# Optimization experiments

Hardware: AMD Instinct MI355X
Metric: run time of the kernel (lower is better)

Reference implementation:

```python
import jax, jax.numpy as jnp
import numpy as np

NLON = 720  # output longitude points for irfft
B, C = 4, 8
LMAX, MMAX, NLAT = 360, 361, 361


def setup_inputs() -> dict:
    key = jax.random.key(0)
    kx, kd = jax.random.split(key)
    # x: real view of complex coeffs, shape [B, C, 2(vec comp), lmax, mmax, 2(re/im)]
    x = jax.random.normal(kx, (B, C, 2, LMAX, MMAX, 2), dtype=jnp.float32)
    # dpct: precomputed dLegendre buffer, shape [2, mmax, lmax, nlat]
    dpct = jax.random.normal(kd, (2, MMAX, LMAX, NLAT), dtype=jnp.float32) * 0.1
    return {"x": x, "dpct": dpct}


def reference(x, dpct):
    # split vector components and real/imag parts
    x0r = x[..., 0, :, :, 0]  # [..., lmax, mmax]
    x0i = x[..., 0, :, :, 1]
    x1r = x[..., 1, :, :, 0]
    x1i = x[..., 1, :, :, 1]
    d0 = dpct[0].astype(x.dtype)  # [mmax, lmax, nlat]
    d1 = dpct[1].astype(x.dtype)

    def ein(a, d):
        return jnp.einsum('...lm,mlk->...km', a, d)

    srl = ein(x0r, d0) - ein(x1i, d1)   # [..., nlat, mmax]
    sim = ein(x0i, d0) + ein(x1r, d1)
    trl = -ein(x0i, d1) - ein(x1r, d0)
    tim = ein(x0r, d1) - ein(x1i, d0)

    s = jax.lax.complex(srl, sim)
    t = jax.lax.complex(trl, tim)
    xs = jnp.stack((s, t), axis=-3)     # [..., 2, nlat, mmax] complex
    # inverse real FFT over longitude, 'forward' norm (no scaling on inverse)
    out = jnp.fft.irfft(xs, n=NLON, axis=-1, norm='forward')  # [..., 2, nlat, nlon]
    return out
```

## Files before the change

kernel.cpp:

```cpp
#include <hip/hip_runtime.h>
#include <hip/hip_bf16.h>
#include <math.h>

#define LMAX 360
#define MMAX 361
#define NLAT 361
#define NLON 720
#define BC   32
#define MT   (BC*2*NLAT)
#define QT   722
#define KP   736
#define NP   768
#define BM   128
#define BN   128
#define BK   32

typedef __attribute__((ext_vector_type(8))) short short8;
typedef __attribute__((ext_vector_type(4))) float f32x4;

static __device__ __forceinline__ short f2bf(float v) {
    __hip_bfloat16 h = __float2bfloat16(v);
    return *reinterpret_cast<short*>(&h);
}

__global__ __launch_bounds__(256) void sht_prep_x(
    const float* __restrict__ x, __hip_bfloat16* __restrict__ xT)
{
    const int m0 = blockIdx.x * 32;
    const int l0 = blockIdx.y * 64;
    const int bc = blockIdx.z >> 1, f = blockIdx.z & 1;
    __shared__ float2 tile[64][33];
    const float2* __restrict__ x2 = (const float2*)x;
    const int t = threadIdx.x;
    const int rm = t & 31, rl = t >> 5;

    const int mm = min(m0 + rm, MMAX - 1);
    #pragma unroll
    for (int r = 0; r < 8; ++r) {
        int l = min(l0 + rl + r * 8, LMAX - 1);
        tile[rl + r * 8][rm] = x2[((size_t)(bc * 2 + f) * LMAX + l) * MMAX + mm];
    }
    __syncthreads();

    const int tm = t >> 3, lg = t & 7;
    const int m = m0 + tm;
    if (m >= MMAX) return;
    const int lw = l0 + lg * 8;
    if (lw >= LMAX) return;

    short8 re, im;
    #pragma unroll
    for (int e = 0; e < 8; ++e) {
        float2 v = tile[lg * 8 + e][tm];
        re[e] = f2bf(v.x);
        im[e] = f2bf(v.y);
    }
    size_t mb = (size_t)m * (128 * LMAX);
    *(short8*)((short*)xT + mb + (size_t)((f * 2 + 0) * 32 + bc) * LMAX + lw) = re;
    *(short8*)((short*)xT + mb + (size_t)((f * 2 + 1) * 32 + bc) * LMAX + lw) = im;
}

__global__ __launch_bounds__(256, 3) void sht_gemm1(
    const float* __restrict__ dpct, const __hip_bfloat16* __restrict__ xT,
    __hip_bfloat16* __restrict__ interQ)
{
    const int m  = blockIdx.x;
    const int K0 = blockIdx.y * 96;

    __shared__ __align__(16) char AlsB[96 * 128];
    __shared__ __align__(16) char BlsB[128 * 128];

    const int t    = threadIdx.x;
    const int lane = t & 63;
    const int wave = t >> 6;
    const int wm = (wave >> 1) * 48;
    const int wn = (wave & 1) * 64;
    const int fr = lane & 15;
    const int lq = lane >> 4;

    int kdv[3], lov[3], kcl[3];
    #pragma unroll
    for (int it = 0; it < 3; ++it) {
        int task = it * 256 + t;
        kdv[it] = task % 96;
        lov[it] = task / 96;
        kcl[it] = min(K0 + kdv[it], 360);
    }
    const int cB    = t >> 1;
    const int plane = cB >> 5, bcq = cB & 31;
    const int g0B   = (t & 1) * 4;

    const int            srcT[8] = {0, 1, 2, 3, 3, 2, 1, 0};
    const unsigned short sgnT[8] = {0, 0, 0x8000, 0x8000, 0x8000, 0, 0x8000, 0};

    f32x4 acc[3][4];
    const f32x4 zero = {0.f, 0.f, 0.f, 0.f};
    #pragma unroll
    for (int i = 0; i < 3; ++i)
        #pragma unroll
        for (int j = 0; j < 4; ++j) acc[i][j] = zero;

    float  apf[3][8];
    short8 bpf[4];
    bool   lvA[3], bvB[4];
    short  bsgn = 0;

    auto loadA = [&](int p, int l0) {
        const size_t rowb = ((size_t)p * MMAX + m) * LMAX;
        #pragma unroll
        for (int it = 0; it < 3; ++it) {
            int lb = l0 + lov[it] * 8;
            lvA[it] = (lb < LMAX);
            int lcl = lvA[it] ? lb : 0;
            const float* src = dpct + (rowb + lcl) * (size_t)NLAT + kcl[it];
            #pragma unroll
            for (int e = 0; e < 8; ++e)
                apf[it][e] = src[(size_t)e * NLAT];
        }
    };

    auto loadB = [&](int p, int l0) {
        int src = srcT[p * 4 + plane];
        bsgn = (short)sgnT[p * 4 + plane];
        const short* bbase = (const short*)xT + (size_t)m * (128 * LMAX) +
                             (size_t)(src * 32 + bcq) * LMAX;
        #pragma unroll
        for (int i = 0; i < 4; ++i) {
            int lg2 = l0 + (g0B + i) * 8;
            bvB[i] = (lg2 < LMAX);
            int lcl = bvB[i] ? lg2 : 0;
            bpf[i] = *(const short8*)(bbase + lcl);
        }
    };

    auto writeA = [&]() {
        #pragma unroll
        for (int it = 0; it < 3; ++it) {
            short8 w;
            #pragma unroll
            for (int e = 0; e < 8; ++e)
                w[e] = lvA[it] ? f2bf(apf[it][e]) : (short)0;
            int kd = kdv[it], lo = lov[it];
            *(short8*)(AlsB + kd * 128 + ((lo ^ (kd & 7)) << 4)) = w;
        }
    };

    auto writeB = [&]() {
        #pragma unroll
        for (int i = 0; i < 4; ++i) {
            short8 v = bpf[i];
            #pragma unroll
            for (int e = 0; e < 8; ++e) {
                short xe = (short)(v[e] ^ bsgn);
                v[e] = bvB[i] ? xe : (short)0;
            }
            int g = g0B + i;
            *(short8*)(BlsB + cB * 128 + ((g ^ (cB & 7)) << 4)) = v;
        }
    };

    loadA(0, 0);
    loadB(0, 0);

    #pragma unroll 1
    for (int s = 0; s < 12; ++s) {
        __syncthreads();
        writeA();
        writeB();
        __syncthreads();

        if (s < 11) {
            const int pn  = (s + 1 >= 6) ? 1 : 0;
            const int l0n = ((s + 1) % 6) * 64;
            loadA(pn, l0n);
            loadB(pn, l0n);
        }

        #pragma unroll
        for (int kk = 0; kk < 2; ++kk) {
            short8 af[3], bg[4];
            const int g = kk * 4 + lq;
            #pragma unroll
            for (int mi = 0; mi < 3; ++mi) {
                int k = wm + mi * 16 + fr;
                af[mi] = *(const short8*)(AlsB + k * 128 + ((g ^ (k & 7)) << 4));
            }
            #pragma unroll
            for (int ni = 0; ni < 4; ++ni) {
                int c = wn + ni * 16 + fr;
                bg[ni] = *(const short8*)(BlsB + c * 128 + ((g ^ (c & 7)) << 4));
            }
            #pragma unroll
            for (int mi = 0; mi < 3; ++mi)
                #pragma unroll
                for (int ni = 0; ni < 4; ++ni)
                    acc[mi][ni] = __builtin_amdgcn_mfma_f32_16x16x32_bf16(
                        af[mi], bg[ni], acc[mi][ni], 0, 0, 0);
        }
    }

    #pragma unroll
    for (int mi = 0; mi < 3; ++mi) {
        int kr = K0 + wm + mi * 16 + lq * 4;
        #pragma unroll
        for (int ni = 0; ni < 4; ++ni) {
            int c = wn + ni * 16 + fr;
            int pl = c >> 5, bc = c & 31;
            int ri = pl & 1, tt = pl >> 1;
            size_t qb = (size_t)(2 * m + ri) * MT + (size_t)(bc * 2 + tt) * NLAT;
            #pragma unroll
            for (int r = 0; r < 4; ++r) {
                int k = kr + r;
                if (k < NLAT)
                    interQ[qb + k] = __float2bfloat16(acc[mi][ni][r]);
            }
        }
    }
}

__global__ __launch_bounds__(256) void sht_transpose(
    const __hip_bfloat16* __restrict__ inQ, __hip_bfloat16* __restrict__ outT)
{
    __shared__ __hip_bfloat16 tile[64][65];
    const int R0 = blockIdx.x * 64;
    const int q0 = blockIdx.y * 64;
    const int tx = threadIdx.x & 63;
    const int ty = threadIdx.x >> 6;
    const __hip_bfloat16 zv = __float2bfloat16(0.f);

    for (int qq = ty; qq < 64; qq += 4) {
        int q = q0 + qq;
        tile[qq][tx] = (q < QT) ? inQ[(size_t)q * MT + R0 + tx] : zv;
    }
    __syncthreads();
    if (q0 + tx < KP) {
        for (int rr = ty; rr < 64; rr += 4) {
            outT[(size_t)(R0 + rr) * KP + q0 + tx] = tile[tx][rr];
        }
    }
}

__global__ __launch_bounds__(256) void sht_make_w(__hip_bfloat16* __restrict__ W)
{
    const int idx = blockIdx.x * 256 + threadIdx.x;
    const int j = idx / KP;
    const int q = idx % KP;
    float v = 0.f;
    if (j < NLON && q < QT) {
        int m = q >> 1;
        float coef = (m == 0 || m == 360) ? 1.f : 2.f;
        int ph = (m * j) % 720;
        float ang = (float)ph * (float)(2.0 * M_PI / 720.0);
        float s, c;
        __sincosf(ang, &s, &c);
        v = (q & 1) ? (-coef * s) : (coef * c);
    }
    W[idx] = __float2bfloat16(v);
}

__global__ __launch_bounds__(256) void sht_gemm(
    const __hip_bfloat16* __restrict__ A,
    const __hip_bfloat16* __restrict__ W,
    float* __restrict__ out)
{
    __shared__ __align__(16) __hip_bfloat16 As[BM * BK];
    __shared__ __align__(16) __hip_bfloat16 Bs[BN * BK];
    const int t  = threadIdx.x;
    const int R0 = blockIdx.x * BM;
    const int J0 = blockIdx.y * BN;

    const int rowA = t >> 2;
    const int kc   = (t & 3) * 8;
    const int gr0  = min(R0 + rowA,      MT - 1);
    const int gr1  = min(R0 + rowA + 64, MT - 1);
    const __hip_bfloat16* pa0 = A + (size_t)gr0 * KP + kc;
    const __hip_bfloat16* pa1 = A + (size_t)gr1 * KP + kc;
    const __hip_bfloat16* pb0 = W + (size_t)(J0 + rowA) * KP + kc;
    const __hip_bfloat16* pb1 = W + (size_t)(J0 + rowA + 64) * KP + kc;

    const int lane = t & 63;
    const int wave = t >> 6;
    const int wm = (wave >> 1) * 64;
    const int wn = (wave & 1) * 64;
    const int fr = lane & 15;
    const int kg = (lane >> 4) * 8;

    f32x4 acc[4][4];
    const f32x4 zero = {0.f, 0.f, 0.f, 0.f};
    #pragma unroll
    for (int i = 0; i < 4; ++i)
        #pragma unroll
        for (int j = 0; j < 4; ++j) acc[i][j] = zero;

    short8 va0 = *(const short8*)pa0;
    short8 va1 = *(const short8*)pa1;
    short8 vb0 = *(const short8*)pb0;
    short8 vb1 = *(const short8*)pb1;

    for (int kt = 0; kt < KP / BK; ++kt) {
        __syncthreads();
        *(short8*)&As[t * 8]        = va0;
        *(short8*)&As[t * 8 + 2048] = va1;
        *(short8*)&Bs[t * 8]        = vb0;
        *(short8*)&Bs[t * 8 + 2048] = vb1;
        __syncthreads();

        if (kt + 1 < KP / BK) {
            const int ko = (kt + 1) * BK;
            va0 = *(const short8*)(pa0 + ko);
            va1 = *(const short8*)(pa1 + ko);
            vb0 = *(const short8*)(pb0 + ko);
            vb1 = *(const short8*)(pb1 + ko);
        }

        short8 af[4], bg[4];
        #pragma unroll
        for (int i = 0; i < 4; ++i)
            af[i] = *(const short8*)&As[(wm + i * 16 + fr) * BK + kg];
        #pragma unroll
        for (int i = 0; i < 4; ++i)
            bg[i] = *(const short8*)&Bs[(wn + i * 16 + fr) * BK + kg];

        #pragma unroll
        for (int mi = 0; mi < 4; ++mi)
            #pragma unroll
            for (int ni = 0; ni < 4; ++ni)
                acc[mi][ni] = __builtin_amdgcn_mfma_f32_16x16x32_bf16(
                    af[mi], bg[ni], acc[mi][ni], 0, 0, 0);
    }

    const int orow = (lane >> 4) * 4;
    #pragma unroll
    for (int mi = 0; mi < 4; ++mi) {
        #pragma unroll
        for (int ni = 0; ni < 4; ++ni) {
            #pragma unroll
            for (int r = 0; r < 4; ++r) {
                int row = R0 + wm + mi * 16 + orow + r;
                int col = J0 + wn + ni * 16 + fr;
                if (row < MT && col < NLON)
                    out[(size_t)row * NLON + col] = acc[mi][ni][r];
            }
        }
    }
}

extern "C" void kernel_launch(void* const* d_in, const int* in_sizes, int n_in,
                              void* d_out, int out_size, void* d_ws, size_t ws_size,
                              hipStream_t stream)
{
    const float* x    = (const float*)d_in[0];
    const float* dpct = (const float*)d_in[1];
    float* out        = (float*)d_out;

    char* ws = (char*)d_ws;
    __hip_bfloat16* xT     = (__hip_bfloat16*)ws;
    __hip_bfloat16* interT = (__hip_bfloat16*)ws;
    __hip_bfloat16* interQ = (__hip_bfloat16*)(ws + 34009088);
    __hip_bfloat16* Wt     = (__hip_bfloat16*)(ws + 34009088);

    dim3 gp(12, 6, 64);
    sht_prep_x<<<gp, 256, 0, stream>>>(x, xT);

    dim3 g1(MMAX, 4);
    sht_gemm1<<<g1, 256, 0, stream>>>(dpct, xT, interQ);

    dim3 gt(MT / 64, 12);
    sht_transpose<<<gt, 256, 0, stream>>>(interQ, interT);

    sht_make_w<<<(NP * KP) / 256, 256, 0, stream>>>(Wt);

    dim3 gg((MT + BM - 1) / BM, NP / BN);
    sht_gemm<<<gg, 256, 0, stream>>>(interT, Wt, out);
}
```

Measured before the change: 273.6 us.

## Pre-convert dpct to padded transposed bf16 layout before the first GEMM

Adds a kernel that reads the fp32 Legendre table, converts it to bf16 and writes it transposed into a zero-padded [p][m][k][l] workspace layout. The first GEMM then loads A tiles as contiguous 16-byte vectors with no per-element conversion or bounds masks, replacing eight strided scalar fp32 loads per thread. Occupancy hint is raised to 4 blocks per CU. This adds a full extra pass over dpct (read fp32, write bf16) every call, so the saving in the GEMM has to exceed the cost of the new kernel.

```diff
diff --git a/kernel.cpp b/kernel.cpp
--- a/kernel.cpp
+++ b/kernel.cpp
@@ -14,6 +14,8 @@
 #define BM   128
 #define BN   128
 #define BK   32
+#define KD4  384
+#define LD4  384
 
 typedef __attribute__((ext_vector_type(8))) short short8;
 typedef __attribute__((ext_vector_type(4))) float f32x4;
@@ -60,8 +62,53 @@
     *(short8*)((short*)xT + mb + (size_t)((f * 2 + 1) * 32 + bc) * LMAX + lw) = im;
 }
 
-__global__ __launch_bounds__(256, 3) void sht_gemm1(
-    const float* __restrict__ dpct, const __hip_bfloat16* __restrict__ xT,
+__global__ __launch_bounds__(256) void sht_conv_dpct(
+    const float* __restrict__ dpct, __hip_bfloat16* __restrict__ dpctT)
+{
+    const int g = blockIdx.x;
+    const int m = blockIdx.y;
+    const int p = blockIdx.z;
+    const int t = threadIdx.x;
+    const bool zpad = (g == 15);
+
+    __shared__ float raw[24 * NLAT];
+
+    if (!zpad) {
+        const float4* __restrict__ src4 = (const float4*)(
+            dpct + ((size_t)(p * MMAX + m) * LMAX + g * 24) * NLAT);
+        float4* raw4 = (float4*)raw;
+        #pragma unroll
+        for (int i = 0; i < 9; ++i) {
+            int idx = i * 256 + t;
+            if (idx < 2166) raw4[idx] = src4[idx];
+        }
+    }
+    __syncthreads();
+
+    short* __restrict__ dstb = (short*)dpctT +
+        ((size_t)(p * MMAX + m) * KD4) * LD4 + g * 24;
+
+    #pragma unroll
+    for (int i = 0; i < 5; ++i) {
+        int task = i * 256 + t;
+        if (task >= 1152) break;
+        int k  = task / 3;
+        int sh = task % 3;
+        short8 w;
+        if (!zpad && k <= 360) {
+            #pragma unroll
+            for (int e = 0; e < 8; ++e)
+                w[e] = f2bf(raw[(sh * 8 + e) * NLAT + k]);
+        } else {
+            #pragma unroll
+            for (int e = 0; e < 8; ++e) w[e] = 0;
+        }
+        *(short8*)(dstb + (size_t)k * LD4 + sh * 8) = w;
+    }
+}
+
+__global__ __launch_bounds__(256, 4) void sht_gemm1(
+    const __hip_bfloat16* __restrict__ dpctT, const __hip_bfloat16* __restrict__ xT,
     __hip_bfloat16* __restrict__ interQ)
 {
     const int m  = blockIdx.x;
@@ -78,13 +125,12 @@
     const int fr = lane & 15;
     const int lq = lane >> 4;
 
-    int kdv[3], lov[3], kcl[3];
+    int kdv[3], lgv[3];
     #pragma unroll
     for (int it = 0; it < 3; ++it) {
         int task = it * 256 + t;
-        kdv[it] = task % 96;
-        lov[it] = task / 96;
-        kcl[it] = min(K0 + kdv[it], 360);
+        kdv[it] = task >> 3;
+        lgv[it] = task & 7;
     }
     const int cB    = t >> 1;
     const int plane = cB >> 5, bcq = cB & 31;
@@ -100,30 +146,25 @@
         #pragma unroll
         for (int j = 0; j < 4; ++j) acc[i][j] = zero;
 
-    float  apf[3][8];
+    short8 apf[3];
     short8 bpf[4];
-    bool   lvA[3], bvB[4];
+    bool   bvB[4];
     short  bsgn = 0;
 
+    const short* __restrict__ abase = (const short*)dpctT;
+    const short* __restrict__ xbase = (const short*)xT + (size_t)m * (128 * LMAX);
+
     auto loadA = [&](int p, int l0) {
-        const size_t rowb = ((size_t)p * MMAX + m) * LMAX;
-        #pragma unroll
-        for (int it = 0; it < 3; ++it) {
-            int lb = l0 + lov[it] * 8;
-            lvA[it] = (lb < LMAX);
-            int lcl = lvA[it] ? lb : 0;
-            const float* src = dpct + (rowb + lcl) * (size_t)NLAT + kcl[it];
-            #pragma unroll
-            for (int e = 0; e < 8; ++e)
-                apf[it][e] = src[(size_t)e * NLAT];
-        }
+        const short* sl = abase + ((size_t)(p * MMAX + m) * KD4 + K0) * LD4 + l0;
+        #pragma unroll
+        for (int it = 0; it < 3; ++it)
+            apf[it] = *(const short8*)(sl + (size_t)kdv[it] * LD4 + lgv[it] * 8);
     };
 
     auto loadB = [&](int p, int l0) {
         int src = srcT[p * 4 + plane];
         bsgn = (short)sgnT[p * 4 + plane];
-        const short* bbase = (const short*)xT + (size_t)m * (128 * LMAX) +
-                             (size_t)(src * 32 + bcq) * LMAX;
+        const short* bbase = xbase + (size_t)(src * 32 + bcq) * LMAX;
         #pragma unroll
         for (int i = 0; i < 4; ++i) {
             int lg2 = l0 + (g0B + i) * 8;
@@ -136,12 +177,8 @@
     auto writeA = [&]() {
         #pragma unroll
         for (int it = 0; it < 3; ++it) {
-            short8 w;
-            #pragma unroll
-            for (int e = 0; e < 8; ++e)
-                w[e] = lvA[it] ? f2bf(apf[it][e]) : (short)0;
-            int kd = kdv[it], lo = lov[it];
-            *(short8*)(AlsB + kd * 128 + ((lo ^ (kd & 7)) << 4)) = w;
+            int kd = kdv[it], lg = lgv[it];
+            *(short8*)(AlsB + kd * 128 + ((lg ^ (kd & 7)) << 4)) = apf[it];
         }
     };
 
@@ -358,12 +395,16 @@
     __hip_bfloat16* interT = (__hip_bfloat16*)ws;
     __hip_bfloat16* interQ = (__hip_bfloat16*)(ws + 34009088);
     __hip_bfloat16* Wt     = (__hip_bfloat16*)(ws + 34009088);
+    __hip_bfloat16* dpctT  = (__hip_bfloat16*)(ws + 67371264);
 
     dim3 gp(12, 6, 64);
     sht_prep_x<<<gp, 256, 0, stream>>>(x, xT);
 
+    dim3 gc(16, MMAX, 2);
+    sht_conv_dpct<<<gc, 256, 0, stream>>>(dpct, dpctT);
+
     dim3 g1(MMAX, 4);
-    sht_gemm1<<<g1, 256, 0, stream>>>(dpct, xT, interQ);
+    sht_gemm1<<<g1, 256, 0, stream>>>(dpctT, xT, interQ);
 
     dim3 gt(MT / 64, 12);
     sht_transpose<<<gt, 256, 0, stream>>>(interQ, interT);
```

Result: slower. 432.5 us (+58.1%).

## Double-buffer register prefetch of A/B tiles two steps ahead in GEMM loop

Applied to the files above, without the earlier changes.

Adds a second set of register staging buffers so global loads for step s+2 are issued while step s is written to LDS and computed, deepening the prefetch from one step to two. The loop is unrolled by two to alternate between the buffers. This aims to hide the strided global loads of dpct behind more MFMA work, at the cost of roughly doubling staging register use, which may reduce occupancy or cause spills.

```diff
diff --git a/kernel.cpp b/kernel.cpp
--- a/kernel.cpp
+++ b/kernel.cpp
@@ -100,12 +100,12 @@
         #pragma unroll
         for (int j = 0; j < 4; ++j) acc[i][j] = zero;
 
-    float  apf[3][8];
-    short8 bpf[4];
-    bool   lvA[3], bvB[4];
-    short  bsgn = 0;
-
-    auto loadA = [&](int p, int l0) {
+    float  apf0[3][8], apf1[3][8];
+    short8 bpf0[4],    bpf1[4];
+    bool   lvA0[3], lvA1[3], bvB0[4], bvB1[4];
+    short  bsgn0 = 0, bsgn1 = 0;
+
+    auto loadA = [&](float (*apf)[8], bool* lvA, int p, int l0) {
         const size_t rowb = ((size_t)p * MMAX + m) * LMAX;
         #pragma unroll
         for (int it = 0; it < 3; ++it) {
@@ -119,7 +119,7 @@
         }
     };
 
-    auto loadB = [&](int p, int l0) {
+    auto loadB = [&](short8* bpf, bool* bvB, short& bsgn, int p, int l0) {
         int src = srcT[p * 4 + plane];
         bsgn = (short)sgnT[p * 4 + plane];
         const short* bbase = (const short*)xT + (size_t)m * (128 * LMAX) +
@@ -133,7 +133,7 @@
         }
     };
 
-    auto writeA = [&]() {
+    auto writeA = [&](const float (*apf)[8], const bool* lvA) {
         #pragma unroll
         for (int it = 0; it < 3; ++it) {
             short8 w;
@@ -145,7 +145,7 @@
         }
     };
 
-    auto writeB = [&]() {
+    auto writeB = [&](const short8* bpf, const bool* bvB, short bsgn) {
         #pragma unroll
         for (int i = 0; i < 4; ++i) {
             short8 v = bpf[i];
@@ -159,23 +159,7 @@
         }
     };
 
-    loadA(0, 0);
-    loadB(0, 0);
-
-    #pragma unroll 1
-    for (int s = 0; s < 12; ++s) {
-        __syncthreads();
-        writeA();
-        writeB();
-        __syncthreads();
-
-        if (s < 11) {
-            const int pn  = (s + 1 >= 6) ? 1 : 0;
-            const int l0n = ((s + 1) % 6) * 64;
-            loadA(pn, l0n);
-            loadB(pn, l0n);
-        }
-
+    auto compute = [&]() {
         #pragma unroll
         for (int kk = 0; kk < 2; ++kk) {
             short8 af[3], bg[4];
@@ -197,7 +181,40 @@
                     acc[mi][ni] = __builtin_amdgcn_mfma_f32_16x16x32_bf16(
                         af[mi], bg[ni], acc[mi][ni], 0, 0, 0);
         }
-    }
+    };
+
+#define STEP_P(s)  ((s) >= 6 ? 1 : 0)
+#define STEP_L(s)  (((s) % 6) * 64)
+
+    loadA(apf0, lvA0, STEP_P(0), STEP_L(0));
+    loadB(bpf0, bvB0, bsgn0, STEP_P(0), STEP_L(0));
+    loadA(apf1, lvA1, STEP_P(1), STEP_L(1));
+    loadB(bpf1, bvB1, bsgn1, STEP_P(1), STEP_L(1));
+
+    #pragma unroll 1
+    for (int s = 0; s < 12; s += 2) {
+        __syncthreads();
+        writeA(apf0, lvA0);
+        writeB(bpf0, bvB0, bsgn0);
+        __syncthreads();
+        if (s + 2 < 12) {
+            loadA(apf0, lvA0, STEP_P(s + 2), STEP_L(s + 2));
+            loadB(bpf0, bvB0, bsgn0, STEP_P(s + 2), STEP_L(s + 2));
+        }
+        compute();
+
+        __syncthreads();
+        writeA(apf1, lvA1);
+        writeB(bpf1, bvB1, bsgn1);
+        __syncthreads();
+        if (s + 3 < 12) {
+            loadA(apf1, lvA1, STEP_P(s + 3), STEP_L(s + 3));
+            loadB(bpf1, bvB1, bsgn1, STEP_P(s + 3), STEP_L(s + 3));
+        }
+        compute();
+    }
+#undef STEP_P
+#undef STEP_L
 
     #pragma unroll
     for (int mi = 0; mi < 3; ++mi) {
```

Result: slower. 889.6 us (+225.2%).
